# Performance work log

Measured on AMD Instinct MI355X. Metric: run time of the kernel, lower is better.

Reference implementation:

```python
import jax, jax.numpy as jnp
import numpy as np

N_NODES = 100000
N_EDGES = 1600000
D_IN = 64
D_OUT = 64


def setup_inputs() -> dict:
    key = jax.random.key(0)
    k1, k2, k3, k4, k5, k6 = jax.random.split(key, 6)
    x = jax.random.normal(k1, (N_NODES, D_IN), dtype=jnp.float32)
    edge_index = jax.random.randint(k2, (2, N_EDGES), 0, N_NODES, dtype=jnp.int64)
    edge_weight = jax.random.uniform(k3, (N_EDGES,), dtype=jnp.float32)
    scale = 1.0 / np.sqrt(D_IN)
    W0 = jax.random.normal(k4, (D_IN, D_OUT), dtype=jnp.float32) * scale
    W1 = jax.random.normal(k5, (D_IN, D_OUT), dtype=jnp.float32) * scale
    b = jax.random.normal(k6, (D_OUT,), dtype=jnp.float32) * 0.01
    return {"x": x, "edge_index": edge_index, "edge_weight": edge_weight,
            "W0": W0, "W1": W1, "b": b}


def reference(x, edge_index, edge_weight, W0, W1, b):
    # ChebConv K=2 with default lambda_max=2.0, sym normalization:
    # L_hat = 2L/lambda_max - I = -D^{-1/2} A D^{-1/2}
    N = x.shape[0]
    row, col = edge_index[0], edge_index[1]
    deg = jax.ops.segment_sum(edge_weight, row, num_segments=N)  # [N]
    deg_safe = jnp.where(deg > 0, deg, 1.0)
    dinv = jnp.where(deg > 0, jax.lax.rsqrt(deg_safe), 0.0)
    norm = -dinv[row] * edge_weight * dinv[col]  # [E], L_hat edge weights
    # Tx_1[i] = sum_{e: col_e = i} norm_e * x[row_e]
    Tx1 = jax.ops.segment_sum(norm[:, None] * x[row], col, num_segments=N)
    # out = lin0(Tx_0) + lin1(Tx_1) + bias
    return x @ W0 + Tx1 @ W1 + b
```

## Files before the change

kernel.cpp:

```cpp
#include <hip/hip_runtime.h>

#define N_NODES 100000
#define N_EDGES 1600000
#define D 64
#define NB 128
#define EPB (N_EDGES / NB)
#define NBUCK 3125
#define NBUCK_PAD 3136
#define NGRP 98
#define CAP 1024
#define ST 68

__global__ __launch_bounds__(512) void count_kernel(const int* __restrict__ row,
                                                    const int* __restrict__ col,
                                                    int* __restrict__ matC,
                                                    int* __restrict__ matR) {
    __shared__ int cC[NBUCK_PAD];
    __shared__ int cR[NBUCK_PAD];
    int t = threadIdx.x;
    for (int j = t; j < NBUCK_PAD; j += 512) { cC[j] = 0; cR[j] = 0; }
    __syncthreads();
    int base = blockIdx.x * EPB;
    for (int i = t; i < EPB; i += 512) {
        int e = base + i;
        atomicAdd(&cC[col[e] >> 5], 1);
        atomicAdd(&cR[row[e] >> 5], 1);
    }
    __syncthreads();
    int* mc = matC + (size_t)blockIdx.x * NBUCK_PAD;
    int* mr = matR + (size_t)blockIdx.x * NBUCK_PAD;
    for (int j = t; j < NBUCK_PAD; j += 512) { mc[j] = cC[j]; mr[j] = cR[j]; }
}

__global__ __launch_bounds__(256) void blockscan_kernel(int* __restrict__ matC,
                                                        int* __restrict__ matR,
                                                        int* __restrict__ totalsC,
                                                        int* __restrict__ totalsR) {
    int which = blockIdx.x / NGRP;
    int grp   = blockIdx.x % NGRP;
    int* mat    = which ? matR : matC;
    int* totals = which ? totalsR : totalsC;
    int j0 = grp * 32;
    __shared__ int tile[NB][33];
    int t = threadIdx.x;
    int r = t >> 1;
    int h = t & 1;
    {
        const int* src = mat + (size_t)r * NBUCK_PAD + j0 + h * 16;
        int4 v0 = *(const int4*)(src + 0);
        int4 v1 = *(const int4*)(src + 4);
        int4 v2 = *(const int4*)(src + 8);
        int4 v3 = *(const int4*)(src + 12);
        int cb = h * 16;
        tile[r][cb+0]=v0.x;  tile[r][cb+1]=v0.y;  tile[r][cb+2]=v0.z;  tile[r][cb+3]=v0.w;
        tile[r][cb+4]=v1.x;  tile[r][cb+5]=v1.y;  tile[r][cb+6]=v1.z;  tile[r][cb+7]=v1.w;
        tile[r][cb+8]=v2.x;  tile[r][cb+9]=v2.y;  tile[r][cb+10]=v2.z; tile[r][cb+11]=v2.w;
        tile[r][cb+12]=v3.x; tile[r][cb+13]=v3.y; tile[r][cb+14]=v3.z; tile[r][cb+15]=v3.w;
    }
    __syncthreads();
    int g = t >> 3;
    int l = t & 7;
    int rows0 = l * 16;
    int vals[16];
    int s = 0;
    #pragma unroll
    for (int i = 0; i < 16; ++i) { vals[i] = tile[rows0 + i][g]; s += vals[i]; }
    int inc = s;
    #pragma unroll
    for (int d = 1; d < 8; d <<= 1) {
        int u = __shfl_up(inc, d, 8);
        if (l >= d) inc += u;
    }
    int excl = inc - s;
    #pragma unroll
    for (int i = 0; i < 16; ++i) { int e2 = excl; excl += vals[i]; tile[rows0 + i][g] = e2; }
    if (l == 7) totals[j0 + g] = inc;
    __syncthreads();
    {
        int* dst = mat + (size_t)r * NBUCK_PAD + j0 + h * 16;
        int cb = h * 16;
        int4 v0 = make_int4(tile[r][cb+0],  tile[r][cb+1],  tile[r][cb+2],  tile[r][cb+3]);
        int4 v1 = make_int4(tile[r][cb+4],  tile[r][cb+5],  tile[r][cb+6],  tile[r][cb+7]);
        int4 v2 = make_int4(tile[r][cb+8],  tile[r][cb+9],  tile[r][cb+10], tile[r][cb+11]);
        int4 v3 = make_int4(tile[r][cb+12], tile[r][cb+13], tile[r][cb+14], tile[r][cb+15]);
        *(int4*)(dst + 0)  = v0;
        *(int4*)(dst + 4)  = v1;
        *(int4*)(dst + 8)  = v2;
        *(int4*)(dst + 12) = v3;
    }
}

__global__ __launch_bounds__(256) void totscan_kernel(const int* __restrict__ totalsC,
                                                      int* __restrict__ bstartC,
                                                      const int* __restrict__ totalsR,
                                                      int* __restrict__ bstartR) {
    const int* tot = blockIdx.x ? totalsR : totalsC;
    int* bst       = blockIdx.x ? bstartR : bstartC;
    const int CH = (NBUCK_PAD + 255) / 256;
    __shared__ int lds[256];
    int t = threadIdx.x;
    int local[CH];
    int s = 0;
    for (int i = 0; i < CH; ++i) {
        int idx = t * CH + i;
        local[i] = (idx < NBUCK_PAD) ? tot[idx] : 0;
        s += local[i];
    }
    lds[t] = s;
    __syncthreads();
    for (int off = 1; off < 256; off <<= 1) {
        int u = (t >= off) ? lds[t - off] : 0;
        __syncthreads();
        lds[t] += u;
        __syncthreads();
    }
    int excl = (t > 0) ? lds[t - 1] : 0;
    for (int i = 0; i < CH; ++i) {
        int idx = t * CH + i;
        if (idx < NBUCK_PAD) bst[idx] = excl;
        excl += local[i];
    }
}

__global__ __launch_bounds__(512) void scatter_kernel(const int* __restrict__ row,
                                                      const int* __restrict__ col,
                                                      const float* __restrict__ w,
                                                      const int* __restrict__ matC,
                                                      const int* __restrict__ matR,
                                                      const int* __restrict__ bstartC,
                                                      const int* __restrict__ bstartR,
                                                      int2* __restrict__ crecs,
                                                      unsigned* __restrict__ rrecs) {
    __shared__ int cursC[NBUCK];
    __shared__ int cursR[NBUCK];
    int t = threadIdx.x;
    const int* offC = matC + (size_t)blockIdx.x * NBUCK_PAD;
    const int* offR = matR + (size_t)blockIdx.x * NBUCK_PAD;
    for (int j = t; j < NBUCK; j += 512) {
        cursC[j] = bstartC[j] + offC[j];
        cursR[j] = bstartR[j] + offR[j];
    }
    __syncthreads();
    int base = blockIdx.x * EPB;
    for (int i = t; i < EPB; i += 512) {
        int e = base + i;
        int r = row[e];
        int c = col[e];
        float we = w[e];
        int pC = atomicAdd(&cursC[c >> 5], 1);
        crecs[pC] = make_int2(r | ((c & 31) << 17), __float_as_int(we));
        int pR = atomicAdd(&cursR[r >> 5], 1);
        rrecs[pR] = (__float_as_uint(we) & ~31u) | (unsigned)(r & 31);
    }
}

__global__ __launch_bounds__(256) void deg_kernel(const unsigned* __restrict__ rrecs,
                                                  const int* __restrict__ bstartR,
                                                  const int* __restrict__ totalsR,
                                                  float* __restrict__ dinv) {
    __shared__ float acc[32];
    int t = threadIdx.x;
    int b = blockIdx.x;
    if (t < 32) acc[t] = 0.f;
    __syncthreads();
    int base = bstartR[b];
    int cnt  = totalsR[b];
    for (int i = t; i < cnt; i += 256) {
        unsigned v = rrecs[base + i];
        atomicAdd(&acc[v & 31u], __uint_as_float(v & ~31u));
    }
    __syncthreads();
    if (t < 32) {
        float d = acc[t];
        dinv[b * 32 + t] = d > 0.f ? rsqrtf(d) : 0.f;
    }
}

#define FMA8(cc, av, bv)                                                       \
    acc0.x += cc * av.x; acc0.y += cc * av.y; acc0.z += cc * av.z; acc0.w += cc * av.w; \
    acc1.x += cc * bv.x; acc1.y += cc * bv.y; acc1.z += cc * bv.z; acc1.w += cc * bv.w;

__global__ __launch_bounds__(256) void gather_out_kernel(
        const int2* __restrict__ crecs, const int* __restrict__ bstartC,
        const int* __restrict__ totalsC, const float* __restrict__ dinv,
        const float* __restrict__ x,
        const float* __restrict__ W0, const float* __restrict__ W1,
        const float* __restrict__ bias, float* __restrict__ out) {
    __shared__ __align__(16) char smem[32 * ST * 4 * 2];
    int2* raw = (int2*)smem;
    int2* srt = (int2*)(smem + 8192);
    int*  cnt32   = (int*)(smem + 16384);
    int*  start32 = cnt32 + 32;
    int*  cur32   = cnt32 + 64;
    float* xs = (float*)smem;
    float* ts = (float*)(smem + 32 * ST * 4);

    int tid = threadIdx.x;
    int b   = blockIdx.x;
    int n0  = b * 32;
    int n   = tid >> 3;
    int j   = tid & 7;

    int base = bstartC[b];
    int cnt  = totalsC[b];

    float4 acc0 = make_float4(0.f, 0.f, 0.f, 0.f);
    float4 acc1 = make_float4(0.f, 0.f, 0.f, 0.f);
    const float* xj = x + (size_t)(j << 3);

    for (int cb = 0; cb < cnt; cb += CAP) {
        int m = min(CAP, cnt - cb);
        if (tid < 32) cnt32[tid] = 0;
        __syncthreads();
        for (int i = tid; i < m; i += 256) {
            int2 rec = crecs[base + cb + i];
            int r = rec.x & 0x1FFFF;
            rec.y = __float_as_int(__int_as_float(rec.y) * dinv[r]);
            raw[i] = rec;
            atomicAdd(&cnt32[((unsigned)rec.x) >> 17], 1);
        }
        __syncthreads();
        if (tid < 32) {
            int v = cnt32[tid];
            int inc = v;
            #pragma unroll
            for (int d = 1; d < 32; d <<= 1) {
                int u = __shfl_up(inc, d, 32);
                if (tid >= d) inc += u;
            }
            start32[tid] = inc - v;
            cur32[tid]   = inc - v;
        }
        __syncthreads();
        for (int i = tid; i < m; i += 256) {
            int2 rec = raw[i];
            int p = atomicAdd(&cur32[((unsigned)rec.x) >> 17], 1);
            srt[p] = rec;
        }
        __syncthreads();
        int ks = start32[n];
        int ke = ks + cnt32[n];
        int k = ks;
        for (; k + 3 < ke; k += 4) {
            int2 e0 = srt[k + 0];
            int2 e1 = srt[k + 1];
            int2 e2 = srt[k + 2];
            int2 e3 = srt[k + 3];
            const float* p0 = xj + (size_t)(e0.x & 0x1FFFF) * D;
            const float* p1 = xj + (size_t)(e1.x & 0x1FFFF) * D;
            const float* p2 = xj + (size_t)(e2.x & 0x1FFFF) * D;
            const float* p3 = xj + (size_t)(e3.x & 0x1FFFF) * D;
            float c0 = __int_as_float(e0.y);
            float c1 = __int_as_float(e1.y);
            float c2 = __int_as_float(e2.y);
            float c3 = __int_as_float(e3.y);
            float4 a0 = *(const float4*)p0, b0 = *(const float4*)(p0 + 4);
            float4 a1 = *(const float4*)p1, b1 = *(const float4*)(p1 + 4);
            float4 a2 = *(const float4*)p2, b2 = *(const float4*)(p2 + 4);
            float4 a3 = *(const float4*)p3, b3 = *(const float4*)(p3 + 4);
            FMA8(c0, a0, b0)
            FMA8(c1, a1, b1)
            FMA8(c2, a2, b2)
            FMA8(c3, a3, b3)
        }
        for (; k < ke; ++k) {
            int2 e0 = srt[k];
            const float* p0 = xj + (size_t)(e0.x & 0x1FFFF) * D;
            float c0 = __int_as_float(e0.y);
            float4 a0 = *(const float4*)p0, b0 = *(const float4*)(p0 + 4);
            FMA8(c0, a0, b0)
        }
        __syncthreads();
    }

    float dn = -dinv[n0 + n];
    float* tp = ts + n * ST + (j << 3);
    *(float4*)tp       = make_float4(dn * acc0.x, dn * acc0.y, dn * acc0.z, dn * acc0.w);
    *(float4*)(tp + 4) = make_float4(dn * acc1.x, dn * acc1.y, dn * acc1.z, dn * acc1.w);
    for (int i = tid; i < 512; i += 256) {
        int nn = i >> 4;
        int kk = (i & 15) << 2;
        *(float4*)&xs[nn * ST + kk] = *(const float4*)(x + (size_t)n0 * D + i * 4);
    }
    __syncthreads();

    int jl = j << 3;
    float4 o0 = *(const float4*)(bias + jl);
    float4 o1 = *(const float4*)(bias + jl + 4);
    for (int k = 0; k < D; k += 4) {
        float4 av = *(const float4*)&xs[n * ST + k];
        float4 tv = *(const float4*)&ts[n * ST + k];
        #pragma unroll
        for (int u = 0; u < 4; ++u) {
            float a = (u == 0) ? av.x : (u == 1) ? av.y : (u == 2) ? av.z : av.w;
            float t = (u == 0) ? tv.x : (u == 1) ? tv.y : (u == 2) ? tv.z : tv.w;
            const float4 w00 = *(const float4*)(W0 + (size_t)(k + u) * D + jl);
            const float4 w01 = *(const float4*)(W0 + (size_t)(k + u) * D + jl + 4);
            const float4 w10 = *(const float4*)(W1 + (size_t)(k + u) * D + jl);
            const float4 w11 = *(const float4*)(W1 + (size_t)(k + u) * D + jl + 4);
            o0.x += a * w00.x + t * w10.x;
            o0.y += a * w00.y + t * w10.y;
            o0.z += a * w00.z + t * w10.z;
            o0.w += a * w00.w + t * w10.w;
            o1.x += a * w01.x + t * w11.x;
            o1.y += a * w01.y + t * w11.y;
            o1.z += a * w01.z + t * w11.z;
            o1.w += a * w01.w + t * w11.w;
        }
    }
    float* op = out + (size_t)(n0 + n) * D + jl;
    *(float4*)op       = o0;
    *(float4*)(op + 4) = o1;
}

extern "C" void kernel_launch(void* const* d_in, const int* in_sizes, int n_in,
                              void* d_out, int out_size, void* d_ws, size_t ws_size,
                              hipStream_t stream) {
    const float* x    = (const float*)d_in[0];
    const int*   eidx = (const int*)d_in[1];
    const float* ew   = (const float*)d_in[2];
    const float* W0   = (const float*)d_in[3];
    const float* W1   = (const float*)d_in[4];
    const float* b    = (const float*)d_in[5];
    float* out = (float*)d_out;

    const int* row = eidx;
    const int* col = eidx + N_EDGES;

    int2*     crecs   = (int2*)d_ws;
    unsigned* rrecs   = (unsigned*)((int*)d_ws + 2 * (size_t)N_EDGES);
    int*      matC    = (int*)rrecs + N_EDGES;
    int*      matR    = matC + (size_t)NB * NBUCK_PAD;
    int*      totalsC = matR + (size_t)NB * NBUCK_PAD;
    int*      bstartC = totalsC + NBUCK_PAD;
    int*      totalsR = bstartC + NBUCK_PAD;
    int*      bstartR = totalsR + NBUCK_PAD;
    float*    dinv    = (float*)(bstartR + NBUCK_PAD);

    count_kernel     <<<NB, 512, 0, stream>>>(row, col, matC, matR);
    blockscan_kernel <<<2 * NGRP, 256, 0, stream>>>(matC, matR, totalsC, totalsR);
    totscan_kernel   <<<2, 256, 0, stream>>>(totalsC, bstartC, totalsR, bstartR);
    scatter_kernel   <<<NB, 512, 0, stream>>>(row, col, ew, matC, matR,
                                              bstartC, bstartR, crecs, rrecs);
    deg_kernel       <<<NBUCK, 256, 0, stream>>>(rrecs, bstartR, totalsR, dinv);
    gather_out_kernel<<<NBUCK, 256, 0, stream>>>(crecs, bstartC, totalsC, dinv,
                                                 x, W0, W1, b, out);
}
```

Measured before the change: 292.5 us.

## Balance edge work evenly across thread groups with LDS atomic flush accumulators

Each 8-thread group no longer owns one destination node. Instead it takes an equal contiguous slice of the sorted edge list and accumulates runs per node in registers. When the destination changes, it flushes the partial sums into a shared-memory accumulator with atomics. This is meant to remove the load imbalance from variable per-node degree, and it also drops the raw staging buffer by re-reading records from global memory in the scatter pass. The cost is extra LDS atomics at segment boundaries, a second global read of the records, and branchy flush logic.

```diff
diff --git a/kernel.cpp b/kernel.cpp
--- a/kernel.cpp
+++ b/kernel.cpp
@@ -9,7 +9,7 @@
 #define NBUCK_PAD 3136
 #define NGRP 98
 #define CAP 1024
-#define ST 68
+#define AST 68
 
 __global__ __launch_bounds__(512) void count_kernel(const int* __restrict__ row,
                                                     const int* __restrict__ col,
@@ -176,9 +176,26 @@
     }
 }
 
-#define FMA8(cc, av, bv)                                                       \
-    acc0.x += cc * av.x; acc0.y += cc * av.y; acc0.z += cc * av.z; acc0.w += cc * av.w; \
-    acc1.x += cc * bv.x; acc1.y += cc * bv.y; acc1.z += cc * bv.z; acc1.w += cc * bv.w;
+#define FLUSH()                                                                \
+    do { if (cur >= 0) {                                                       \
+        float* ap = accL + cur * AST + (j << 3);                               \
+        atomicAdd(ap + 0, a0.x); atomicAdd(ap + 1, a0.y);                      \
+        atomicAdd(ap + 2, a0.z); atomicAdd(ap + 3, a0.w);                      \
+        atomicAdd(ap + 4, a1.x); atomicAdd(ap + 5, a1.y);                      \
+        atomicAdd(ap + 6, a1.z); atomicAdd(ap + 7, a1.w);                      \
+    }                                                                          \
+    a0 = make_float4(0.f,0.f,0.f,0.f); a1 = make_float4(0.f,0.f,0.f,0.f);      \
+    } while (0)
+
+#define PROC(e, v0, v1)                                                        \
+    do { int nd = ((unsigned)(e).x) >> 17;                                     \
+        if (nd != cur) { FLUSH(); cur = nd; }                                  \
+        float cc = __int_as_float((e).y);                                      \
+        a0.x += cc * (v0).x; a0.y += cc * (v0).y;                              \
+        a0.z += cc * (v0).z; a0.w += cc * (v0).w;                              \
+        a1.x += cc * (v1).x; a1.y += cc * (v1).y;                              \
+        a1.z += cc * (v1).z; a1.w += cc * (v1).w;                              \
+    } while (0)
 
 __global__ __launch_bounds__(256) void gather_out_kernel(
         const int2* __restrict__ crecs, const int* __restrict__ bstartC,
@@ -186,39 +203,33 @@
         const float* __restrict__ x,
         const float* __restrict__ W0, const float* __restrict__ W1,
         const float* __restrict__ bias, float* __restrict__ out) {
-    __shared__ __align__(16) char smem[32 * ST * 4 * 2];
-    int2* raw = (int2*)smem;
-    int2* srt = (int2*)(smem + 8192);
-    int*  cnt32   = (int*)(smem + 16384);
-    int*  start32 = cnt32 + 32;
-    int*  cur32   = cnt32 + 64;
-    float* xs = (float*)smem;
-    float* ts = (float*)(smem + 32 * ST * 4);
+    __shared__ __align__(16) char smemA[32 * AST * 4];
+    __shared__ __align__(16) char smemB[32 * AST * 4];
+    __shared__ int cnt32[32];
+    __shared__ int cur32[32];
+    int2*  srt  = (int2*)smemA;
+    float* xs   = (float*)smemA;
+    float* accL = (float*)smemB;
+    float* ts   = accL;
 
     int tid = threadIdx.x;
     int b   = blockIdx.x;
     int n0  = b * 32;
-    int n   = tid >> 3;
+    int g   = tid >> 3;
     int j   = tid & 7;
+
+    for (int i = tid; i < 32 * AST; i += 256) accL[i] = 0.f;
 
     int base = bstartC[b];
     int cnt  = totalsC[b];
-
-    float4 acc0 = make_float4(0.f, 0.f, 0.f, 0.f);
-    float4 acc1 = make_float4(0.f, 0.f, 0.f, 0.f);
     const float* xj = x + (size_t)(j << 3);
 
     for (int cb = 0; cb < cnt; cb += CAP) {
         int m = min(CAP, cnt - cb);
         if (tid < 32) cnt32[tid] = 0;
         __syncthreads();
-        for (int i = tid; i < m; i += 256) {
-            int2 rec = crecs[base + cb + i];
-            int r = rec.x & 0x1FFFF;
-            rec.y = __float_as_int(__int_as_float(rec.y) * dinv[r]);
-            raw[i] = rec;
-            atomicAdd(&cnt32[((unsigned)rec.x) >> 17], 1);
-        }
+        for (int i = tid; i < m; i += 256)
+            atomicAdd(&cnt32[((unsigned)crecs[base + cb + i].x) >> 17], 1);
         __syncthreads();
         if (tid < 32) {
             int v = cnt32[tid];
@@ -228,20 +239,26 @@
                 int u = __shfl_up(inc, d, 32);
                 if (tid >= d) inc += u;
             }
-            start32[tid] = inc - v;
-            cur32[tid]   = inc - v;
+            cur32[tid] = inc - v;
         }
         __syncthreads();
         for (int i = tid; i < m; i += 256) {
-            int2 rec = raw[i];
+            int2 rec = crecs[base + cb + i];
+            int r = rec.x & 0x1FFFF;
+            rec.y = __float_as_int(__int_as_float(rec.y) * dinv[r]);
             int p = atomicAdd(&cur32[((unsigned)rec.x) >> 17], 1);
             srt[p] = rec;
         }
         __syncthreads();
-        int ks = start32[n];
-        int ke = ks + cnt32[n];
-        int k = ks;
-        for (; k + 3 < ke; k += 4) {
+        int q   = m >> 5;
+        int rem = m & 31;
+        int lo  = g * q + (g < rem ? g : rem);
+        int hi  = lo + q + (g < rem ? 1 : 0);
+        float4 a0 = make_float4(0.f,0.f,0.f,0.f);
+        float4 a1 = make_float4(0.f,0.f,0.f,0.f);
+        int cur = -1;
+        int k = lo;
+        for (; k + 3 < hi; k += 4) {
             int2 e0 = srt[k + 0];
             int2 e1 = srt[k + 1];
             int2 e2 = srt[k + 2];
@@ -250,37 +267,39 @@
             const float* p1 = xj + (size_t)(e1.x & 0x1FFFF) * D;
             const float* p2 = xj + (size_t)(e2.x & 0x1FFFF) * D;
             const float* p3 = xj + (size_t)(e3.x & 0x1FFFF) * D;
-            float c0 = __int_as_float(e0.y);
-            float c1 = __int_as_float(e1.y);
-            float c2 = __int_as_float(e2.y);
-            float c3 = __int_as_float(e3.y);
-            float4 a0 = *(const float4*)p0, b0 = *(const float4*)(p0 + 4);
-            float4 a1 = *(const float4*)p1, b1 = *(const float4*)(p1 + 4);
-            float4 a2 = *(const float4*)p2, b2 = *(const float4*)(p2 + 4);
-            float4 a3 = *(const float4*)p3, b3 = *(const float4*)(p3 + 4);
-            FMA8(c0, a0, b0)
-            FMA8(c1, a1, b1)
-            FMA8(c2, a2, b2)
-            FMA8(c3, a3, b3)
-        }
-        for (; k < ke; ++k) {
+            float4 v00 = *(const float4*)p0, v01 = *(const float4*)(p0 + 4);
+            float4 v10 = *(const float4*)p1, v11 = *(const float4*)(p1 + 4);
+            float4 v20 = *(const float4*)p2, v21 = *(const float4*)(p2 + 4);
+            float4 v30 = *(const float4*)p3, v31 = *(const float4*)(p3 + 4);
+            PROC(e0, v00, v01);
+            PROC(e1, v10, v11);
+            PROC(e2, v20, v21);
+            PROC(e3, v30, v31);
+        }
+        for (; k < hi; ++k) {
             int2 e0 = srt[k];
             const float* p0 = xj + (size_t)(e0.x & 0x1FFFF) * D;
-            float c0 = __int_as_float(e0.y);
-            float4 a0 = *(const float4*)p0, b0 = *(const float4*)(p0 + 4);
-            FMA8(c0, a0, b0)
-        }
-        __syncthreads();
-    }
-
-    float dn = -dinv[n0 + n];
-    float* tp = ts + n * ST + (j << 3);
-    *(float4*)tp       = make_float4(dn * acc0.x, dn * acc0.y, dn * acc0.z, dn * acc0.w);
-    *(float4*)(tp + 4) = make_float4(dn * acc1.x, dn * acc1.y, dn * acc1.z, dn * acc1.w);
+            float4 v00 = *(const float4*)p0, v01 = *(const float4*)(p0 + 4);
+            PROC(e0, v00, v01);
+        }
+        FLUSH();
+        __syncthreads();
+    }
+
+    {
+        float dn = -dinv[n0 + g];
+        float* tp = ts + g * AST + (j << 3);
+        float4 t0 = *(float4*)tp;
+        float4 t1 = *(float4*)(tp + 4);
+        t0.x *= dn; t0.y *= dn; t0.z *= dn; t0.w *= dn;
+        t1.x *= dn; t1.y *= dn; t1.z *= dn; t1.w *= dn;
+        *(float4*)tp       = t0;
+        *(float4*)(tp + 4) = t1;
+    }
     for (int i = tid; i < 512; i += 256) {
         int nn = i >> 4;
         int kk = (i & 15) << 2;
-        *(float4*)&xs[nn * ST + kk] = *(const float4*)(x + (size_t)n0 * D + i * 4);
+        *(float4*)&xs[nn * AST + kk] = *(const float4*)(x + (size_t)n0 * D + i * 4);
     }
     __syncthreads();
 
@@ -288,8 +307,8 @@
     float4 o0 = *(const float4*)(bias + jl);
     float4 o1 = *(const float4*)(bias + jl + 4);
     for (int k = 0; k < D; k += 4) {
-        float4 av = *(const float4*)&xs[n * ST + k];
-        float4 tv = *(const float4*)&ts[n * ST + k];
+        float4 av = *(const float4*)&xs[g * AST + k];
+        float4 tv = *(const float4*)&ts[g * AST + k];
         #pragma unroll
         for (int u = 0; u < 4; ++u) {
             float a = (u == 0) ? av.x : (u == 1) ? av.y : (u == 2) ? av.z : av.w;
@@ -308,7 +327,7 @@
             o1.w += a * w01.w + t * w11.w;
         }
     }
-    float* op = out + (size_t)(n0 + n) * D + jl;
+    float* op = out + (size_t)(n0 + g) * D + jl;
     *(float4*)op       = o0;
     *(float4*)(op + 4) = o1;
 }
```

After: 296.3 us. Within noise of the previous version (+1.3%).
